# Performance work log

Measured on AMD Instinct MI355X. Metric: run time of the kernel, lower is better.

## Reference

```python
import jax, jax.numpy as jnp
import numpy as np

# Static problem sizes (see shape_source)
B, D, H, W = 2, 16, 64, 64          # batch, sparse_shape = grid_size[::-1]
NV = 20000                           # active voxels per batch sample
CIN = 16                             # input_channels
THRESH = 0.5                         # FOCAL_THRESHOLD (used for kernel-offset mask)
EPS = 1e-3                           # BatchNorm eps from norm_fn
K_FORE = int(NV * THRESH)            # topk split: top int(N*threshold) voxels are foreground
# kernel_offsets: [[i,j,k] for i,j,k in (-1..1)^3] minus [0,0,0], applied to [z,y,x]
OFFSETS = [(i, j, k) for i in range(-1, 2) for j in range(-1, 2) for k in range(-1, 2) if (i, j, k) != (0, 0, 0)]


def _conv(x, w):
    # dense 3x3x3 conv == SubMConv3d math at active sites (inactive cells hold zeros)
    return jax.lax.conv_general_dilated(x, w, (1, 1, 1), 'SAME',
                                        dimension_numbers=('NDHWC', 'DHWIO', 'NDHWC'))


def _bn(x, g, b, m, v):
    # eval-mode BatchNorm1d over voxel features
    return (x - m) * (g * jax.lax.rsqrt(v + EPS)) + b


def setup_inputs() -> dict:
    rng = np.random.default_rng(0)
    coords = []
    for b in range(B):  # unique voxel coords per sample (spconv requires unique indices)
        lin = rng.permutation(D * H * W)[:NV]
        z = lin // (H * W); r = lin % (H * W)
        coords.append(np.stack([np.full(NV, b), z, r // W, r % W], 1))
    voxel_coords = jnp.asarray(np.concatenate(coords, 0), jnp.int32)  # [B*NV, 4] = [b,z,y,x]
    ks = jax.random.split(jax.random.key(0), 24)

    def bn_p(i, c):
        return (1.0 + 0.1 * jax.random.normal(ks[i], (c,)),
                0.1 * jax.random.normal(ks[i + 1], (c,)),
                0.1 * jax.random.normal(ks[i + 2], (c,)),
                jax.random.uniform(ks[i + 3], (c,), minval=0.5, maxval=1.5))

    g1, b1, m1, v1 = bn_p(4, 32)
    g2, b2, m2, v2 = bn_p(8, 64)
    g3, b3, m3, v3 = bn_p(12, 128)
    return dict(
        voxel_features=jax.random.normal(ks[0], (B * NV, CIN), jnp.float32),
        voxel_coords=voxel_coords,
        w1=0.08 * jax.random.normal(ks[1], (3, 3, 3, CIN, 32), jnp.float32),
        w2=0.06 * jax.random.normal(ks[2], (3, 3, 3, 32, 64), jnp.float32),
        w_imp=0.05 * jax.random.normal(ks[3], (3, 3, 3, 64, 27), jnp.float32),
        w_focal=0.04 * jax.random.normal(ks[16], (3, 3, 3, 64, 128), jnp.float32),
        g1=g1, b1=b1, m1=m1, v1=v1,
        g2=g2, b2=b2, m2=m2, v2=v2,
        g3=g3, b3=b3, m3=m3, v3=v3)


def reference(voxel_features, w1, g1, b1, m1, v1, w2, g2, b2, m2, v2,
              w_imp, w_focal, g3, b3, m3, v3, voxel_coords):
    bi, z, y, x = (voxel_coords[:, i] for i in range(4))
    # scatter sparse voxels into dense grid; zeros at inactive cells
    dense = jnp.zeros((B, D, H, W, CIN), voxel_features.dtype).at[bi, z, y, x].set(voxel_features)
    active = jnp.zeros((B, D, H, W), bool).at[bi, z, y, x].set(True)
    am = active[..., None].astype(voxel_features.dtype)

    # conv_input: two SubMConv3d + BN + ReLU (re-mask so inactive cells stay zero)
    h = jax.nn.relu(_bn(_conv(dense, w1), g1, b1, m1, v1)) * am   # -> 32
    h = jax.nn.relu(_bn(_conv(h, w2), g2, b2, m2, v2)) * am       # -> 64

    # conv_imp -> 27 logits; last = voxel importance, first 26 = kernel-offset importances
    imp = _conv(h, w_imp)
    mask_voxel = jax.nn.sigmoid(imp[..., -1])
    mask_kernel = jax.nn.sigmoid(imp[..., :26])

    # split_voxels with topk=True: foreground = top int(NV*thr) voxels per batch by importance
    mv_flat = jnp.where(active, mask_voxel, -jnp.inf).reshape(B, -1)
    kth = jax.lax.top_k(mv_flat, K_FORE)[0][:, -1]
    fore = active & (mask_voxel >= kth[:, None, None, None])

    # dilate foreground by kernel offsets where offset importance >= threshold.
    # New voxels carry zero features; check_repeat (index_add dedup) then reduces to:
    # final features == original features, final actives == active OR dilated candidates.
    new_act = active
    for i, (oz, oy, ox) in enumerate(OFFSETS):
        src = fore & (mask_kernel[..., i] >= THRESH)
        p = jnp.pad(src, ((0, 0), (1, 1), (1, 1), (1, 1)))  # zero(False)-pad for shift
        sh = p[:, 1 - oz:1 - oz + D, 1 - oy:1 - oy + H, 1 - ox:1 - ox + W]
        # original bound check is strict (>0), so plane 0 of each axis is invalid
        sh = sh.at[:, 0].set(False).at[:, :, 0].set(False).at[:, :, :, 0].set(False)
        new_act = new_act | sh

    # conv_focal on merged sparse set (new voxels have zero features -> dense conv matches)
    out = jax.nn.relu(_bn(_conv(h, w_focal), g3, b3, m3, v3)) * new_act[..., None].astype(h.dtype)
    return out  # densified encoded_spconv_tensor features [B, D, H, W, 128]
```

## Files before the change

kernel.cpp:

```cpp
#include <hip/hip_runtime.h>
#include <stdint.h>

#define Dd 16
#define Hh 64
#define Ww 64
#define NACT 40000
#define NVb 20000
#define KFORE 10000
#define EPSf 0.001f

typedef __attribute__((ext_vector_type(8))) short short8;
typedef __attribute__((ext_vector_type(4))) float f32x4;
typedef __attribute__((ext_vector_type(4))) unsigned short us4;

static __device__ __forceinline__ uint32_t f2sort(float f) {
    uint32_t u = __float_as_uint(f);
    return (u & 0x80000000u) ? ~u : (u | 0x80000000u);
}

static __device__ __forceinline__ unsigned short f2b(float f) {
    uint32_t u = __float_as_uint(f);
    return (unsigned short)((u + 0x7FFFu + ((u >> 16) & 1u)) >> 16);
}

static __device__ __forceinline__ int xcd_swz(int orig, int nwg) {
    int xcd = orig & 7, idx = orig >> 3;
    int q = nwg >> 3, r = nwg & 7;
    int base = xcd < r ? xcd * (q + 1) : r * (q + 1) + (xcd - r) * q;
    return base + idx;
}

__global__ void __launch_bounds__(256) k_scatter(const float* __restrict__ feat,
                                                 const int* __restrict__ coords,
                                                 float* __restrict__ dense16,
                                                 uint8_t* __restrict__ active,
                                                 uint8_t* __restrict__ new_act) {
    int i = blockIdx.x * 256 + threadIdx.x;
    if (i >= NACT) return;
    int b = coords[i * 4 + 0], z = coords[i * 4 + 1], y = coords[i * 4 + 2], x = coords[i * 4 + 3];
    int pos = ((b * Dd + z) * Hh + y) * Ww + x;
    active[pos] = 1;
    new_act[pos] = 1;
    const float4* f4 = (const float4*)(feat + (size_t)i * 16);
    float4* d4 = (float4*)(dense16 + (size_t)pos * 16);
    d4[0] = f4[0]; d4[1] = f4[1]; d4[2] = f4[2]; d4[3] = f4[3];
}

__global__ void __launch_bounds__(256) k_cnt(const uint8_t* __restrict__ mask,
                                             int* __restrict__ bcnt) {
    __shared__ int s[256];
    const int i = blockIdx.x * 256 + threadIdx.x;
    s[threadIdx.x] = mask[i] ? 1 : 0;
    __syncthreads();
    for (int off = 128; off > 0; off >>= 1) {
        if (threadIdx.x < off) s[threadIdx.x] += s[threadIdx.x + off];
        __syncthreads();
    }
    if (threadIdx.x == 0) bcnt[blockIdx.x] = s[0];
}

__global__ void __launch_bounds__(512) k_scan(const int* __restrict__ bcnt,
                                              int* __restrict__ boff, int* __restrict__ count) {
    __shared__ int s[512];
    const int t = threadIdx.x;
    const int v0 = bcnt[t];
    s[t] = v0;
    __syncthreads();
    for (int off = 1; off < 512; off <<= 1) {
        int v = s[t];
        if (t >= off) v += s[t - off];
        __syncthreads();
        s[t] = v;
        __syncthreads();
    }
    boff[t] = s[t] - v0;
    if (t == 511) *count = s[511];
}

__global__ void __launch_bounds__(256) k_emit(const uint8_t* __restrict__ mask,
                                              const int* __restrict__ boff,
                                              int* __restrict__ list) {
    __shared__ int s[256];
    const int i = blockIdx.x * 256 + threadIdx.x;
    const int pred = mask[i] ? 1 : 0;
    s[threadIdx.x] = pred;
    __syncthreads();
    for (int off = 1; off < 256; off <<= 1) {
        int v = s[threadIdx.x];
        if (threadIdx.x >= off) v += s[threadIdx.x - off];
        __syncthreads();
        s[threadIdx.x] = v;
        __syncthreads();
    }
    if (pred) list[boff[blockIdx.x] + s[threadIdx.x] - 1] = i;
}

__global__ void __launch_bounds__(256) k_conv1p(const int* __restrict__ list,
        const float* __restrict__ dense16, const float* __restrict__ w1,
        float* __restrict__ pbuf) {
    const int gb = xcd_swz(blockIdx.x, 157 * 12);
    const int chunk = gb / 12, sub = gb % 12;
    const int tp = sub >> 2, cb = (sub & 3) * 8;
    const int i = chunk * 256 + threadIdx.x;
    if (i >= NACT) return;
    const int pos = list[i];
    const int z = (pos >> 12) & 15, y = (pos >> 6) & 63, x = pos & 63;
    float acc[8];
    #pragma unroll
    for (int c = 0; c < 8; ++c) acc[c] = 0.f;
    const int dz = tp - 1;
    if ((unsigned)(z + dz) < Dd) {
        for (int tt = 0; tt < 9; ++tt) {
            const int dy = tt / 3 - 1, dx = tt % 3 - 1;
            if (!((unsigned)(y + dy) < Hh && (unsigned)(x + dx) < Ww)) continue;
            const float* row = dense16 + (size_t)(pos + dz * 4096 + dy * 64 + dx) * 16;
            const float* wt = w1 + (tp * 9 + tt) * 512 + cb;
            #pragma unroll
            for (int k4 = 0; k4 < 4; ++k4) {
                float4 xv = *(const float4*)(row + k4 * 4);
                float xs[4] = {xv.x, xv.y, xv.z, xv.w};
                #pragma unroll
                for (int j = 0; j < 4; ++j)
                    #pragma unroll
                    for (int c = 0; c < 8; ++c)
                        acc[c] = fmaf(xs[j], wt[(k4 * 4 + j) * 32 + c], acc[c]);
            }
        }
    }
    #pragma unroll
    for (int c = 0; c < 8; ++c) pbuf[(size_t)(tp * 32 + cb + c) * NACT + i] = acc[c];
}

__global__ void __launch_bounds__(256) k_conv1c(const int* __restrict__ list,
        const float* __restrict__ pbuf,
        const float* __restrict__ g, const float* __restrict__ bta,
        const float* __restrict__ mu, const float* __restrict__ va,
        float* __restrict__ h1) {
    const int i = blockIdx.x * 256 + threadIdx.x;
    if (i >= NACT) return;
    const int pos = list[i];
    float res[32];
    #pragma unroll
    for (int c = 0; c < 32; ++c) {
        float s = pbuf[(size_t)c * NACT + i]
                + pbuf[(size_t)(32 + c) * NACT + i]
                + pbuf[(size_t)(64 + c) * NACT + i];
        const float sc = g[c] * (1.0f / sqrtf(va[c] + EPSf));
        res[c] = fmaxf(0.f, fmaf(s - mu[c], sc, bta[c]));
    }
    #pragma unroll
    for (int c4 = 0; c4 < 8; ++c4)
        *(float4*)(h1 + (size_t)pos * 32 + c4 * 4) = *(float4*)&res[c4 * 4];
}

__global__ void __launch_bounds__(256) k_conv2p(const int* __restrict__ list,
        const float* __restrict__ h1, const float* __restrict__ w2,
        float* __restrict__ pbuf) {
    const int gb = xcd_swz(blockIdx.x, 157 * 12);
    const int chunk = gb / 12, sub = gb % 12;
    const int tp = sub >> 2, cb = (sub & 3) * 16;
    const int i = chunk * 256 + threadIdx.x;
    if (i >= NACT) return;
    const int pos = list[i];
    const int z = (pos >> 12) & 15, y = (pos >> 6) & 63, x = pos & 63;
    float acc[16];
    #pragma unroll
    for (int c = 0; c < 16; ++c) acc[c] = 0.f;
    const int dz = tp - 1;
    if ((unsigned)(z + dz) < Dd) {
        for (int tt = 0; tt < 9; ++tt) {
            const int dy = tt / 3 - 1, dx = tt % 3 - 1;
            if (!((unsigned)(y + dy) < Hh && (unsigned)(x + dx) < Ww)) continue;
            const float* row = h1 + (size_t)(pos + dz * 4096 + dy * 64 + dx) * 32;
            const float* wt = w2 + (tp * 9 + tt) * 2048 + cb;
            #pragma unroll
            for (int k4 = 0; k4 < 8; ++k4) {
                float4 xv = *(const float4*)(row + k4 * 4);
                float xs[4] = {xv.x, xv.y, xv.z, xv.w};
                #pragma unroll
                for (int j = 0; j < 4; ++j)
                    #pragma unroll
                    for (int c = 0; c < 16; ++c)
                        acc[c] = fmaf(xs[j], wt[(k4 * 4 + j) * 64 + c], acc[c]);
            }
        }
    }
    #pragma unroll
    for (int c = 0; c < 16; ++c) pbuf[(size_t)(tp * 64 + cb + c) * NACT + i] = acc[c];
}

__global__ void __launch_bounds__(256) k_conv2c(const int* __restrict__ list,
        const float* __restrict__ pbuf,
        const float* __restrict__ g, const float* __restrict__ bta,
        const float* __restrict__ mu, const float* __restrict__ va,
        float* __restrict__ h2, unsigned short* __restrict__ h2b) {
    const int i = blockIdx.x * 256 + threadIdx.x;
    if (i >= NACT) return;
    const int pos = list[i];
    float res[64];
    #pragma unroll
    for (int c = 0; c < 64; ++c) {
        float s = pbuf[(size_t)c * NACT + i]
                + pbuf[(size_t)(64 + c) * NACT + i]
                + pbuf[(size_t)(128 + c) * NACT + i];
        const float sc = g[c] * (1.0f / sqrtf(va[c] + EPSf));
        res[c] = fmaxf(0.f, fmaf(s - mu[c], sc, bta[c]));
    }
    #pragma unroll
    for (int c4 = 0; c4 < 16; ++c4)
        *(float4*)(h2 + (size_t)pos * 64 + c4 * 4) = *(float4*)&res[c4 * 4];
    #pragma unroll
    for (int c4 = 0; c4 < 16; ++c4) {
        us4 o = { f2b(res[c4 * 4]), f2b(res[c4 * 4 + 1]), f2b(res[c4 * 4 + 2]), f2b(res[c4 * 4 + 3]) };
        *(us4*)(h2b + (size_t)pos * 64 + c4 * 4) = o;
    }
}

template<int CB, int NC>
static __device__ __forceinline__ void imp_part(int i, int pos, int tp,
        const float* __restrict__ h2, const float* __restrict__ wimp,
        float* __restrict__ pbuf) {
    const int z = (pos >> 12) & 15, y = (pos >> 6) & 63, x = pos & 63;
    float acc[NC];
    #pragma unroll
    for (int c = 0; c < NC; ++c) acc[c] = 0.f;
    for (int tt = 0; tt < 3; ++tt) {
        const int t = tp * 3 + tt;
        const int dz = t / 9 - 1, dy = (t / 3) % 3 - 1, dx = t % 3 - 1;
        if (!((unsigned)(z + dz) < Dd && (unsigned)(y + dy) < Hh && (unsigned)(x + dx) < Ww)) continue;
        const float* row = h2 + (size_t)(pos + dz * 4096 + dy * 64 + dx) * 64;
        const float* wt = wimp + t * 1728 + CB;
        #pragma unroll
        for (int k4 = 0; k4 < 16; ++k4) {
            float4 xv = *(const float4*)(row + k4 * 4);
            float xs[4] = {xv.x, xv.y, xv.z, xv.w};
            #pragma unroll
            for (int j = 0; j < 4; ++j)
                #pragma unroll
                for (int c = 0; c < NC; ++c)
                    acc[c] = fmaf(xs[j], wt[(k4 * 4 + j) * 27 + c], acc[c]);
        }
    }
    #pragma unroll
    for (int c = 0; c < NC; ++c) pbuf[(size_t)(tp * 27 + CB + c) * NACT + i] = acc[c];
}

__global__ void __launch_bounds__(256) k_impp(const int* __restrict__ list,
        const float* __restrict__ h2, const float* __restrict__ wimp,
        float* __restrict__ pbuf) {
    const int gb = xcd_swz(blockIdx.x, 157 * 18);
    const int chunk = gb / 18, sub = gb % 18;
    const int tp = sub >> 1;
    const int i = chunk * 256 + threadIdx.x;
    if (i >= NACT) return;
    const int pos = list[i];
    if (sub & 1) imp_part<14, 13>(i, pos, tp, h2, wimp, pbuf);
    else         imp_part<0, 14>(i, pos, tp, h2, wimp, pbuf);
}

__global__ void __launch_bounds__(256) k_impc(const float* __restrict__ pbuf,
        uint32_t* __restrict__ u_logits, uint32_t* __restrict__ kbits) {
    const int i = blockIdx.x * 256 + threadIdx.x;
    if (i >= NACT) return;
    uint32_t bits = 0;
    float logit = 0.f;
    #pragma unroll
    for (int c = 0; c < 27; ++c) {
        float s = 0.f;
        #pragma unroll
        for (int tp = 0; tp < 9; ++tp)
            s += pbuf[(size_t)(tp * 27 + c) * NACT + i];
        if (c < 26) bits |= (s >= 0.f ? 1u : 0u) << c;
        else logit = s;
    }
    kbits[i] = bits;
    u_logits[i] = f2sort(logit);
}

__global__ void __launch_bounds__(256) k_select(const uint32_t* __restrict__ u_all,
                                                uint32_t* __restrict__ kth_u) {
    const int b = blockIdx.x;
    const uint32_t* u = u_all + (size_t)b * NVb;
    __shared__ int hist[256];
    __shared__ int s_d, s_above;
    uint32_t prefix = 0;
    int K = KFORE;
    for (int p = 3; p >= 0; --p) {
        hist[threadIdx.x] = 0;
        __syncthreads();
        const int sh = p * 8;
        for (int i = threadIdx.x; i < NVb; i += 256) {
            uint32_t ui = u[i];
            bool cand;
            if (p == 3) cand = true;
            else cand = ((ui >> (sh + 8)) == prefix);
            if (cand) atomicAdd(&hist[(ui >> sh) & 255], 1);
        }
        __syncthreads();
        if (threadIdx.x == 0) {
            int cum = 0, d = 255;
            for (; d >= 0; --d) { cum += hist[d]; if (cum >= K) break; }
            s_d = d; s_above = cum - hist[d];
        }
        __syncthreads();
        prefix = (prefix << 8) | (uint32_t)s_d;
        K -= s_above;
        __syncthreads();
    }
    if (threadIdx.x == 0) kth_u[b] = prefix;
}

__global__ void __launch_bounds__(256) k_dilate(const int* __restrict__ list,
                                                const uint32_t* __restrict__ u_logits,
                                                const uint32_t* __restrict__ kbits,
                                                const uint32_t* __restrict__ kth_u,
                                                uint8_t* __restrict__ new_act) {
    int i = blockIdx.x * 256 + threadIdx.x;
    if (i >= NACT) return;
    int pos = list[i];
    int b = pos >> 16;
    if (u_logits[i] < kth_u[b]) return;
    int z = (pos >> 12) & 15, y = (pos >> 6) & 63, x = pos & 63;
    uint32_t bits = kbits[i];
    while (bits) {
        int ch = __ffs(bits) - 1;
        bits &= bits - 1;
        int l = ch + (ch >= 13 ? 1 : 0);
        int oz = l / 9 - 1, oy = (l / 3) % 3 - 1, ox = l % 3 - 1;
        int tz = z + oz, ty = y + oy, tx = x + ox;
        if (tz >= 1 && tz < Dd && ty >= 1 && ty < Hh && tx >= 1 && tx < Ww)
            new_act[((b * Dd + tz) * Hh + ty) * Ww + tx] = 1;
    }
}

__global__ void __launch_bounds__(256) k_zero(const uint8_t* __restrict__ new_act,
                                              float* __restrict__ out) {
    const int pos = blockIdx.x * 256 + threadIdx.x;
    if (new_act[pos]) return;
    float4 z = {0.f, 0.f, 0.f, 0.f};
    float4* o = (float4*)(out + (size_t)pos * 128);
    #pragma unroll
    for (int j = 0; j < 32; ++j) o[j] = z;
}

__global__ void __launch_bounds__(256) k_wcvt(const float* __restrict__ wf,
                                              unsigned short* __restrict__ wfb) {
    int i = blockIdx.x * 256 + threadIdx.x;
    int t = i >> 13, r = i & 8191, n = r >> 6, k = r & 63;
    wfb[i] = f2b(wf[(t * 64 + k) * 128 + n]);
}

__global__ void __launch_bounds__(256, 4) k_focal(
        const int* __restrict__ list, const int* __restrict__ count,
        const unsigned short* __restrict__ h2b, const unsigned short* __restrict__ wfb,
        const float* __restrict__ g, const float* __restrict__ bta,
        const float* __restrict__ mu, const float* __restrict__ va,
        float* __restrict__ out, const unsigned short* __restrict__ zb) {
    __shared__ __align__(16) unsigned short As[3][64 * 64];
    __shared__ int s_pos[64];
    const int n = *count;
    const int i0 = xcd_swz(blockIdx.x, 2048) * 64;
    if (i0 >= n) return;
    const int tid = threadIdx.x;
    const int wv = tid >> 6, lane = tid & 63;
    if (tid < 64) { int idx = i0 + tid; s_pos[tid] = idx < n ? list[idx] : -1; }
    __syncthreads();
    const int v0 = tid >> 3, c8 = tid & 7, v1 = v0 + 32;
    const int p0 = s_pos[v0], p1 = s_pos[v1];
    const int z0 = (p0 >> 12) & 15, y0 = (p0 >> 6) & 63, x0 = p0 & 63;
    const int z1 = (p1 >> 12) & 15, y1 = (p1 >> 6) & 63, x1 = p1 & 63;
    const int wslot = (c8 ^ (v0 & 7)) << 3;
    const int wa0 = v0 * 64 + wslot, wa1 = v1 * 64 + wslot;
    const int hi = lane >> 4, lo = lane & 15;
    const int cb = wv * 32;

    f32x4 acc[4][2];
    #pragma unroll
    for (int mi = 0; mi < 4; ++mi)
        #pragma unroll
        for (int ni = 0; ni < 2; ++ni) acc[mi][ni] = (f32x4){0.f, 0.f, 0.f, 0.f};

    auto gather = [&](int t, short8& r0, short8& r1) {
        int dz = t / 9 - 1, dy = (t / 3) % 3 - 1, dx = t % 3 - 1;
        int off = dz * 4096 + dy * 64 + dx;
        bool ok0 = p0 >= 0 && (unsigned)(z0 + dz) < Dd && (unsigned)(y0 + dy) < Hh && (unsigned)(x0 + dx) < Ww;
        bool ok1 = p1 >= 0 && (unsigned)(z1 + dz) < Dd && (unsigned)(y1 + dy) < Hh && (unsigned)(x1 + dx) < Ww;
        r0 = *(const short8*)(ok0 ? h2b + (size_t)(p0 + off) * 64 + c8 * 8 : zb);
        r1 = *(const short8*)(ok1 ? h2b + (size_t)(p1 + off) * 64 + c8 * 8 : zb);
    };

    auto load_w = [&](int t, short8 (&w)[2][2]) {
        #pragma unroll
        for (int ni = 0; ni < 2; ++ni)
            #pragma unroll
            for (int ks = 0; ks < 2; ++ks)
                w[ni][ks] = *(const short8*)(wfb + (size_t)t * 8192
                                + (size_t)(cb + ni * 16 + lo) * 64 + ks * 32 + hi * 8);
    };

    auto compute = [&](int buf, const short8 (&w)[2][2]) {
        #pragma unroll
        for (int ks = 0; ks < 2; ++ks) {
            const int rs = ((ks * 4 + hi) ^ (lo & 7)) << 3;
            short8 a[4];
            #pragma unroll
            for (int mi = 0; mi < 4; ++mi)
                a[mi] = *(const short8*)&As[buf][(mi * 16 + lo) * 64 + rs];
            #pragma unroll
            for (int mi = 0; mi < 4; ++mi)
                #pragma unroll
                for (int ni = 0; ni < 2; ++ni)
                    acc[mi][ni] = __builtin_amdgcn_mfma_f32_16x16x32_bf16(
                        a[mi], w[ni][ks], acc[mi][ni], 0, 0, 0);
        }
    };

    short8 rA0, rA1, rB0, rB1;
    short8 wE[2][2], wO[2][2];
    gather(0, rA0, rA1);
    gather(1, rB0, rB1);
    *(short8*)&As[0][wa0] = rA0; *(short8*)&As[0][wa1] = rA1;
    *(short8*)&As[1][wa0] = rB0; *(short8*)&As[1][wa1] = rB1;
    gather(2, rA0, rA1);
    gather(3, rB0, rB1);
    load_w(0, wE);
    load_w(1, wO);
    __syncthreads();

    for (int t = 0; t < 27; t += 2) {
        compute(t % 3, wE);
        if (t + 2 < 27) load_w(t + 2, wE);
        if (t + 2 < 27) {
            *(short8*)&As[(t + 2) % 3][wa0] = rA0;
            *(short8*)&As[(t + 2) % 3][wa1] = rA1;
            if (t + 4 < 27) gather(t + 4, rA0, rA1);
        }
        __syncthreads();
        if (t + 1 >= 27) break;
        compute((t + 1) % 3, wO);
        if (t + 3 < 27) load_w(t + 3, wO);
        if (t + 3 < 27) {
            *(short8*)&As[(t + 3) % 3][wa0] = rB0;
            *(short8*)&As[(t + 3) % 3][wa1] = rB1;
            if (t + 5 < 27) gather(t + 5, rB0, rB1);
        }
        __syncthreads();
    }

    #pragma unroll
    for (int ni = 0; ni < 2; ++ni) {
        const int ch = cb + ni * 16 + lo;
        const float s = g[ch] * (1.0f / sqrtf(va[ch] + EPSf));
        const float sh = bta[ch], mm = mu[ch];
        #pragma unroll
        for (int mi = 0; mi < 4; ++mi)
            #pragma unroll
            for (int j = 0; j < 4; ++j) {
                int vi = mi * 16 + hi * 4 + j;
                if (i0 + vi < n)
                    out[(size_t)s_pos[vi] * 128 + ch] = fmaxf(0.f, fmaf(acc[mi][ni][j] - mm, s, sh));
            }
    }
}

extern "C" void kernel_launch(void* const* d_in, const int* in_sizes, int n_in,
                              void* d_out, int out_size, void* d_ws, size_t ws_size,
                              hipStream_t stream) {
    (void)in_sizes; (void)n_in; (void)ws_size; (void)out_size;
    const float* feat   = (const float*)d_in[0];
    const int*   coords = (const int*)d_in[1];
    const float* w1   = (const float*)d_in[2];
    const float* w2   = (const float*)d_in[3];
    const float* wimp = (const float*)d_in[4];
    const float* wf   = (const float*)d_in[5];
    const float* g1 = (const float*)d_in[6],  *b1 = (const float*)d_in[7];
    const float* m1 = (const float*)d_in[8],  *v1 = (const float*)d_in[9];
    const float* g2 = (const float*)d_in[10], *b2 = (const float*)d_in[11];
    const float* m2 = (const float*)d_in[12], *v2 = (const float*)d_in[13];
    const float* g3 = (const float*)d_in[14], *b3 = (const float*)d_in[15];
    const float* m3 = (const float*)d_in[16], *v3 = (const float*)d_in[17];

    char* ws = (char*)d_ws;
    float*    dense16  = (float*)(ws + 0);
    float*    h1       = (float*)(ws + 8388608);
    float*    h2       = (float*)(ws + 25165824);
    uint8_t*  active   = (uint8_t*)(ws + 58720256);
    uint8_t*  new_act  = (uint8_t*)(ws + 58851328);
    float*    zrow     = (float*)(ws + 58982400);
    int*      count    = (int*)(ws + 58982656);
    const size_t MEMSET_BYTES = 58982912;
    uint32_t* u_logits = (uint32_t*)(ws + 58982912);
    uint32_t* kbits    = (uint32_t*)(ws + 59142912);
    uint32_t* kth_u    = (uint32_t*)(ws + 59302912);
    int*      list     = (int*)(ws + 59303168);

    unsigned short* wfb = (unsigned short*)dense16;
    unsigned short* h2b = (unsigned short*)h1;
    float* pbuf = (float*)d_out;
    int* bcnt = (int*)kbits;
    int* boff = (int*)kbits + 512;

    hipMemsetAsync(d_ws, 0, MEMSET_BYTES, stream);

    k_scatter<<<157, 256, 0, stream>>>(feat, coords, dense16, active, new_act);
    k_cnt<<<512, 256, 0, stream>>>(active, bcnt);
    k_scan<<<1, 512, 0, stream>>>(bcnt, boff, count);
    k_emit<<<512, 256, 0, stream>>>(active, boff, list);
    k_conv1p<<<157 * 12, 256, 0, stream>>>(list, dense16, w1, pbuf);
    k_conv1c<<<157, 256, 0, stream>>>(list, pbuf, g1, b1, m1, v1, h1);
    k_wcvt<<<864, 256, 0, stream>>>(wf, wfb);
    k_conv2p<<<157 * 12, 256, 0, stream>>>(list, h1, w2, pbuf);
    hipMemsetAsync(h2b, 0, (size_t)131072 * 64 * 2, stream);
    k_conv2c<<<157, 256, 0, stream>>>(list, pbuf, g2, b2, m2, v2, h2, h2b);
    k_impp<<<157 * 18, 256, 0, stream>>>(list, h2, wimp, pbuf);
    k_impc<<<157, 256, 0, stream>>>(pbuf, u_logits, kbits);
    k_select<<<2, 256, 0, stream>>>(u_logits, kth_u);
    k_dilate<<<157, 256, 0, stream>>>(list, u_logits, kbits, kth_u, new_act);
    k_zero<<<512, 256, 0, stream>>>(new_act, (float*)d_out);
    k_cnt<<<512, 256, 0, stream>>>(new_act, bcnt);
    k_scan<<<1, 512, 0, stream>>>(bcnt, boff, count);
    k_emit<<<512, 256, 0, stream>>>(new_act, boff, list);
    k_focal<<<2048, 256, 0, stream>>>(list, count, h2b, wfb, g3, b3, m3, v3,
                                      (float*)d_out, (const unsigned short*)zrow);
}
```

Before: 527.9 us.

## Load focal-conv A operands directly from global memory, dropping LDS staging

The focal conv kernel no longer stages gathered neighbor features through a triple-buffered shared-memory tile with barriers. Each wave now computes neighbor pointers for its own MFMA rows and loads A fragments straight from global memory, relying on the compiler to pipeline across a loop unrolled by 3. This removes the LDS traffic, the barriers and the shared-memory footprint, which could raise occupancy. The cost is that each of the 4 waves redundantly fetches the same activation rows and loses the explicit software prefetch, leaving it to the cache hierarchy.

Result: slower. 705.2 us (+33.6%).

```diff
diff --git a/kernel.cpp b/kernel.cpp
--- a/kernel.cpp
+++ b/kernel.cpp
@@ -356,7 +356,6 @@
         const float* __restrict__ g, const float* __restrict__ bta,
         const float* __restrict__ mu, const float* __restrict__ va,
         float* __restrict__ out, const unsigned short* __restrict__ zb) {
-    __shared__ __align__(16) unsigned short As[3][64 * 64];
     __shared__ int s_pos[64];
     const int n = *count;
     const int i0 = xcd_swz(blockIdx.x, 2048) * 64;
@@ -365,47 +364,48 @@
     const int wv = tid >> 6, lane = tid & 63;
     if (tid < 64) { int idx = i0 + tid; s_pos[tid] = idx < n ? list[idx] : -1; }
     __syncthreads();
-    const int v0 = tid >> 3, c8 = tid & 7, v1 = v0 + 32;
-    const int p0 = s_pos[v0], p1 = s_pos[v1];
-    const int z0 = (p0 >> 12) & 15, y0 = (p0 >> 6) & 63, x0 = p0 & 63;
-    const int z1 = (p1 >> 12) & 15, y1 = (p1 >> 6) & 63, x1 = p1 & 63;
-    const int wslot = (c8 ^ (v0 & 7)) << 3;
-    const int wa0 = v0 * 64 + wslot, wa1 = v1 * 64 + wslot;
     const int hi = lane >> 4, lo = lane & 15;
     const int cb = wv * 32;
 
+    int pm[4], zm[4], ym[4], xm[4];
+    #pragma unroll
+    for (int mi = 0; mi < 4; ++mi) {
+        pm[mi] = s_pos[mi * 16 + lo];
+        zm[mi] = (pm[mi] >> 12) & 15;
+        ym[mi] = (pm[mi] >> 6) & 63;
+        xm[mi] = pm[mi] & 63;
+    }
+
     f32x4 acc[4][2];
     #pragma unroll
     for (int mi = 0; mi < 4; ++mi)
         #pragma unroll
         for (int ni = 0; ni < 2; ++ni) acc[mi][ni] = (f32x4){0.f, 0.f, 0.f, 0.f};
 
-    auto gather = [&](int t, short8& r0, short8& r1) {
-        int dz = t / 9 - 1, dy = (t / 3) % 3 - 1, dx = t % 3 - 1;
-        int off = dz * 4096 + dy * 64 + dx;
-        bool ok0 = p0 >= 0 && (unsigned)(z0 + dz) < Dd && (unsigned)(y0 + dy) < Hh && (unsigned)(x0 + dx) < Ww;
-        bool ok1 = p1 >= 0 && (unsigned)(z1 + dz) < Dd && (unsigned)(y1 + dy) < Hh && (unsigned)(x1 + dx) < Ww;
-        r0 = *(const short8*)(ok0 ? h2b + (size_t)(p0 + off) * 64 + c8 * 8 : zb);
-        r1 = *(const short8*)(ok1 ? h2b + (size_t)(p1 + off) * 64 + c8 * 8 : zb);
-    };
-
-    auto load_w = [&](int t, short8 (&w)[2][2]) {
+    #pragma unroll 3
+    for (int t = 0; t < 27; ++t) {
+        const int dz = t / 9 - 1, dy = (t / 3) % 3 - 1, dx = t % 3 - 1;
+        const int off = dz * 4096 + dy * 64 + dx;
+        const unsigned short* bp[4];
+        #pragma unroll
+        for (int mi = 0; mi < 4; ++mi) {
+            bool ok = pm[mi] >= 0 && (unsigned)(zm[mi] + dz) < Dd
+                      && (unsigned)(ym[mi] + dy) < Hh && (unsigned)(xm[mi] + dx) < Ww;
+            bp[mi] = ok ? h2b + (size_t)(pm[mi] + off) * 64 : zb;
+        }
+        short8 w[2][2];
         #pragma unroll
         for (int ni = 0; ni < 2; ++ni)
             #pragma unroll
             for (int ks = 0; ks < 2; ++ks)
                 w[ni][ks] = *(const short8*)(wfb + (size_t)t * 8192
                                 + (size_t)(cb + ni * 16 + lo) * 64 + ks * 32 + hi * 8);
-    };
-
-    auto compute = [&](int buf, const short8 (&w)[2][2]) {
         #pragma unroll
         for (int ks = 0; ks < 2; ++ks) {
-            const int rs = ((ks * 4 + hi) ^ (lo & 7)) << 3;
             short8 a[4];
             #pragma unroll
             for (int mi = 0; mi < 4; ++mi)
-                a[mi] = *(const short8*)&As[buf][(mi * 16 + lo) * 64 + rs];
+                a[mi] = *(const short8*)(bp[mi] + ks * 32 + hi * 8);
             #pragma unroll
             for (int mi = 0; mi < 4; ++mi)
                 #pragma unroll
@@ -413,38 +413,6 @@
                     acc[mi][ni] = __builtin_amdgcn_mfma_f32_16x16x32_bf16(
                         a[mi], w[ni][ks], acc[mi][ni], 0, 0, 0);
         }
-    };
-
-    short8 rA0, rA1, rB0, rB1;
-    short8 wE[2][2], wO[2][2];
-    gather(0, rA0, rA1);
-    gather(1, rB0, rB1);
-    *(short8*)&As[0][wa0] = rA0; *(short8*)&As[0][wa1] = rA1;
-    *(short8*)&As[1][wa0] = rB0; *(short8*)&As[1][wa1] = rB1;
-    gather(2, rA0, rA1);
-    gather(3, rB0, rB1);
-    load_w(0, wE);
-    load_w(1, wO);
-    __syncthreads();
-
-    for (int t = 0; t < 27; t += 2) {
-        compute(t % 3, wE);
-        if (t + 2 < 27) load_w(t + 2, wE);
-        if (t + 2 < 27) {
-            *(short8*)&As[(t + 2) % 3][wa0] = rA0;
-            *(short8*)&As[(t + 2) % 3][wa1] = rA1;
-            if (t + 4 < 27) gather(t + 4, rA0, rA1);
-        }
-        __syncthreads();
-        if (t + 1 >= 27) break;
-        compute((t + 1) % 3, wO);
-        if (t + 3 < 27) load_w(t + 3, wO);
-        if (t + 3 < 27) {
-            *(short8*)&As[(t + 3) % 3][wa0] = rB0;
-            *(short8*)&As[(t + 3) % 3][wa1] = rB1;
-            if (t + 5 < 27) gather(t + 5, rB0, rB1);
-        }
-        __syncthreads();
     }
 
     #pragma unroll
```
